# Kernel tuning notes

Hardware: AMD Instinct MI355X
Metric: run time of the kernel (lower is better)

The kernel has to match this reference:

```python
import jax, jax.numpy as jnp
import numpy as np

N_WAY = 100
K_SHOT = 10
N_SUPPORT = N_WAY * K_SHOT
N_QUERY = 8192
F_IN = 4096
D_EMB = 1024
EPS = 1e-6  # torch nn.PairwiseDistance default eps added to the difference


def setup_inputs() -> dict:
    key = jax.random.key(0)
    k1, k2, k3, k4 = jax.random.split(key, 4)
    support_images = jax.random.normal(k1, (N_SUPPORT, F_IN), dtype=jnp.float32)
    # dense labels 0..N_WAY-1, K_SHOT examples each (episodic sampling)
    support_labels = (jnp.arange(N_SUPPORT, dtype=jnp.int32) // K_SHOT)
    query_images = jax.random.normal(k2, (N_QUERY, F_IN), dtype=jnp.float32)
    W = jax.random.normal(k3, (F_IN, D_EMB), dtype=jnp.float32) * (1.0 / np.sqrt(F_IN))
    b = jax.random.normal(k4, (D_EMB,), dtype=jnp.float32) * 0.01
    return {"support_images": support_images, "support_labels": support_labels,
            "query_images": query_images, "W": W, "b": b}


def reference(support_images, support_labels, query_images, W, b):
    # backbone: linear feature extractor
    z_support = support_images @ W + b          # [N_SUPPORT, D]
    z_query = query_images @ W + b              # [N_QUERY, D]

    # group support embeddings by class (each class has exactly K_SHOT members)
    order = jnp.argsort(support_labels, stable=True)
    grouped = z_support[order].reshape(N_WAY, K_SHOT, D_EMB)  # [W, K, D]

    # torch .median(dim=0): lower median for even counts -> sorted[(K-1)//2]
    z_proto_med = jnp.sort(grouped, axis=1)[:, (K_SHOT - 1) // 2]  # [W, D]
    z_proto_mean = grouped.mean(axis=1)                            # [W, D]
    z_total = 0.5 * (z_proto_med + z_proto_mean)                   # [W, D]

    # pairwise L2 with torch PairwiseDistance eps: sqrt(sum((q - p + eps)^2))
    # expanded: ||q||^2 + ||p||^2 + D*eps^2 - 2 q.p + 2*eps*(sum q - sum p)
    q2 = jnp.sum(z_query * z_query, axis=-1, keepdims=True)       # [Q, 1]
    p2 = jnp.sum(z_total * z_total, axis=-1)[None, :]             # [1, W]
    qs = jnp.sum(z_query, axis=-1, keepdims=True)                 # [Q, 1]
    ps = jnp.sum(z_total, axis=-1)[None, :]                       # [1, W]
    cross = z_query @ z_total.T                                   # [Q, W]
    sq = q2 + p2 - 2.0 * cross + 2.0 * EPS * (qs - ps) + D_EMB * EPS * EPS
    dists = jnp.sqrt(jnp.maximum(sq, 0.0))                        # [Q, W]
    return -dists
```

## Files before the change

kernel.cpp:

```cpp
#include <hip/hip_runtime.h>


typedef unsigned short u16;
typedef __attribute__((ext_vector_type(4))) unsigned short u16x4;
typedef __attribute__((ext_vector_type(8))) unsigned short u16x8;
typedef __attribute__((ext_vector_type(8))) short bf16x8;
typedef __attribute__((ext_vector_type(4))) float f32x4;

#define N_QUERY 8192
#define F_IN    4096
#define D_EMB   1024
#define N_SUP   1000
#define N_WAY   100
#define BK      64
#define BM      96

__device__ __forceinline__ u16 f2b(float f) {
  unsigned int u = __builtin_bit_cast(unsigned int, f);
  u += 0x7FFFu + ((u >> 16) & 1u);
  return (u16)(u >> 16);
}
__device__ __forceinline__ float b2f(u16 u) {
  unsigned int x = ((unsigned int)u) << 16;
  return __builtin_bit_cast(float, x);
}

#define GLB_PTR(p) ((const __attribute__((address_space(1))) unsigned int*)(p))
#define LDS_PTR(p) ((__attribute__((address_space(3))) unsigned int*)(p))

__global__ __launch_bounds__(256) void wt_k(const float* __restrict__ W,
                                            u16* __restrict__ Wt) {
  __shared__ float tile[32][33];
  int kb = blockIdx.x * 32, nb = blockIdx.y * 32;
  int tx = threadIdx.x & 31, ty = threadIdx.x >> 5;
#pragma unroll
  for (int i = 0; i < 4; ++i) {
    int k = ty + i * 8;
    tile[k][tx] = W[(size_t)(kb + k) * D_EMB + nb + tx];
  }
  __syncthreads();
#pragma unroll
  for (int i = 0; i < 4; ++i) {
    int n = ty + i * 8;
    Wt[(size_t)(nb + n) * F_IN + kb + tx] = f2b(tile[tx][n]);
  }
}

__global__ __launch_bounds__(512) void gemm1_k(
    const float* __restrict__ qimg, const float* __restrict__ simg,
    const u16* __restrict__ Wt, const float* __restrict__ bias,
    u16* __restrict__ Zq) {
  __shared__ __align__(16) u16 As[BM * BK];
  __shared__ __align__(16) u16 Bs[128 * BK];
  const int tid  = threadIdx.x;
  const int lane = tid & 63, wid = tid >> 6;
  const int wr = wid >> 2, wc = wid & 3;
  int lin = blockIdx.x + (blockIdx.y << 3);
  int swz = (lin & 7) * 96 + (lin >> 3);
  const int rowBase = (swz >> 3) * BM;
  const int colBase = (swz & 7) * 128;
  const bool a2 = (tid < 256);

  const float* asrc[2];
  int aw[2];
#pragma unroll
  for (int i = 0; i < 2; ++i) {
    int g = i * 512 + tid;
    if (g > 767) g = 767;
    int row = g >> 3;
    int colb = ((g & 7) << 4) ^ ((row & 7) << 4);
    int grow = rowBase + row;
    int sr = grow - N_QUERY; if (sr < 0) sr = 0; if (sr > N_SUP - 1) sr = N_SUP - 1;
    const float* base = (grow < N_QUERY) ? qimg + (size_t)grow * F_IN
                                         : simg + (size_t)sr * F_IN;
    asrc[i] = base + (colb >> 1);
    aw[i] = g * 8;
  }
  const u16* bsrc[2];
  unsigned bldsoff[2];
#pragma unroll
  for (int i = 0; i < 2; ++i) {
    int g = i * 512 + tid;
    int n = g >> 3;
    int kb = ((g & 7) << 4) ^ ((n & 7) << 4);
    bsrc[i] = Wt + (size_t)(colBase + n) * F_IN + (kb >> 1);
    bldsoff[i] = i * 8192 + wid * 1024;
  }
  int aoff[3], boff[2];
#pragma unroll
  for (int m = 0; m < 3; ++m) {
    int row = wr * 48 + m * 16 + (lane & 15);
    aoff[m] = (row * 128 + (((lane >> 4) << 4) ^ ((row & 7) << 4))) >> 1;
  }
#pragma unroll
  for (int n = 0; n < 2; ++n) {
    int row = wc * 32 + n * 16 + (lane & 15);
    boff[n] = (row * 128 + (((lane >> 4) << 4) ^ ((row & 7) << 4))) >> 1;
  }

  f32x4 acc[3][2] = {};

#pragma unroll 1
  for (int kt = 0; kt < F_IN / BK; ++kt) {
    float4 v0a = *(const float4*)(asrc[0] + kt * BK);
    float4 v0b = *(const float4*)(asrc[0] + kt * BK + 4);
    float4 v1a = {}, v1b = {};
    if (a2) {
      v1a = *(const float4*)(asrc[1] + kt * BK);
      v1b = *(const float4*)(asrc[1] + kt * BK + 4);
    }
#pragma unroll
    for (int i = 0; i < 2; ++i)
      __builtin_amdgcn_global_load_lds(GLB_PTR(bsrc[i] + kt * BK),
                                       LDS_PTR((char*)Bs + bldsoff[i]), 16, 0, 0);
    u16x8 pk0 = { f2b(v0a.x), f2b(v0a.y), f2b(v0a.z), f2b(v0a.w),
                  f2b(v0b.x), f2b(v0b.y), f2b(v0b.z), f2b(v0b.w) };
    *(u16x8*)&As[aw[0]] = pk0;
    if (a2) {
      u16x8 pk1 = { f2b(v1a.x), f2b(v1a.y), f2b(v1a.z), f2b(v1a.w),
                    f2b(v1b.x), f2b(v1b.y), f2b(v1b.z), f2b(v1b.w) };
      *(u16x8*)&As[aw[1]] = pk1;
    }
    __syncthreads();

#pragma unroll
    for (int ks = 0; ks < 2; ++ks) {
      bf16x8 a[3], b[2];
#pragma unroll
      for (int m = 0; m < 3; ++m) a[m] = *(const bf16x8*)&As[aoff[m] ^ (ks << 5)];
#pragma unroll
      for (int n = 0; n < 2; ++n) b[n] = *(const bf16x8*)&Bs[boff[n] ^ (ks << 5)];
#pragma unroll
      for (int m = 0; m < 3; ++m)
#pragma unroll
        for (int n = 0; n < 2; ++n)
          acc[m][n] = __builtin_amdgcn_mfma_f32_16x16x32_bf16(a[m], b[n], acc[m][n], 0, 0, 0);
    }
    __syncthreads();
  }

#pragma unroll
  for (int n = 0; n < 2; ++n) {
    int c = colBase + wc * 32 + n * 16 + (lane & 15);
    float bvv = bias[c];
#pragma unroll
    for (int m = 0; m < 3; ++m) {
      int r0 = rowBase + wr * 48 + m * 16 + ((lane >> 4) * 4);
#pragma unroll
      for (int r = 0; r < 4; ++r)
        Zq[(size_t)(r0 + r) * D_EMB + c] = f2b(acc[m][n][r] + bvv);
    }
  }
}

__global__ __launch_bounds__(256) void proto_k(const u16* __restrict__ Zq,
                                               float* __restrict__ Ztf) {
  int gid = blockIdx.x * 256 + threadIdx.x;
  int w = gid >> 10, d = gid & 1023;
  float outv = 0.f;
  if (w < N_WAY) {
    float v[10]; float s = 0.f;
#pragma unroll
    for (int k = 0; k < 10; ++k) {
      v[k] = b2f(Zq[(size_t)(N_QUERY + w * 10 + k) * D_EMB + d]);
      s += v[k];
    }
#pragma unroll
    for (int a = 0; a < 9; ++a)
#pragma unroll
      for (int b2 = 0; b2 < 9; ++b2)
        if (b2 < 9 - a) {
          float lo = fminf(v[b2], v[b2 + 1]);
          float hi = fmaxf(v[b2], v[b2 + 1]);
          v[b2] = lo; v[b2 + 1] = hi;
        }
    outv = 0.5f * (v[4] + s * 0.1f);
  }
  Ztf[gid] = outv;
}

__global__ __launch_bounds__(256) void statsq_k(const u16* __restrict__ Zq,
                                                float* __restrict__ sum2,
                                                float* __restrict__ sum1) {
  int row = blockIdx.x;
  int t = threadIdx.x;
  u16x4 u = *(const u16x4*)(Zq + (size_t)row * D_EMB + t * 4);
  float x0 = b2f(u[0]), x1 = b2f(u[1]), x2 = b2f(u[2]), x3 = b2f(u[3]);
  float s  = x0 + x1 + x2 + x3;
  float s2 = x0 * x0 + x1 * x1 + x2 * x2 + x3 * x3;
#pragma unroll
  for (int o = 32; o > 0; o >>= 1) {
    s  += __shfl_down(s, o);
    s2 += __shfl_down(s2, o);
  }
  __shared__ float as1[4], as2[4];
  if ((t & 63) == 0) { as1[t >> 6] = s; as2[t >> 6] = s2; }
  __syncthreads();
  if (t == 0) {
    sum1[row] = as1[0] + as1[1] + as1[2] + as1[3];
    sum2[row] = as2[0] + as2[1] + as2[2] + as2[3];
  }
}

__global__ __launch_bounds__(256) void stats_k(const float* __restrict__ in,
                                               u16* __restrict__ outb,
                                               float* __restrict__ sum2,
                                               float* __restrict__ sum1) {
  int row = blockIdx.x;
  const float* r = in + (size_t)row * D_EMB;
  int t = threadIdx.x;
  float4 v = *(const float4*)(r + t * 4);
  u16x4 u4 = { f2b(v.x), f2b(v.y), f2b(v.z), f2b(v.w) };
  *(u16x4*)(outb + (size_t)row * D_EMB + t * 4) = u4;
  float s  = v.x + v.y + v.z + v.w;
  float s2 = v.x * v.x + v.y * v.y + v.z * v.z + v.w * v.w;
#pragma unroll
  for (int off = 32; off > 0; off >>= 1) {
    s  += __shfl_down(s, off);
    s2 += __shfl_down(s2, off);
  }
  __shared__ float as1[4], as2[4];
  if ((t & 63) == 0) { as1[t >> 6] = s; as2[t >> 6] = s2; }
  __syncthreads();
  if (t == 0) {
    sum1[row] = as1[0] + as1[1] + as1[2] + as1[3];
    sum2[row] = as2[0] + as2[1] + as2[2] + as2[3];
  }
}

#define LDA2 40
__global__ __launch_bounds__(256) void gemm2_k(
    const u16* __restrict__ Zq, const u16* __restrict__ Ztb,
    const float* __restrict__ q2, const float* __restrict__ qs,
    const float* __restrict__ p2, const float* __restrict__ ps,
    float* __restrict__ out) {
  __shared__ u16 As[64][LDA2];
  __shared__ u16 Bs[128][LDA2];
  const int tid = threadIdx.x;
  const int lane = tid & 63, wid = tid >> 6;
  const int wr = wid >> 1, wc = wid & 1;
  const int rowBase = blockIdx.x * 64;

  f32x4 acc[2][4] = {};

  for (int kt = 0; kt < D_EMB / 32; ++kt) {
    u16x8 avv;
    {
      int row = tid >> 2, kh = tid & 3;
      avv = *(const u16x8*)(Zq + (size_t)(rowBase + row) * D_EMB + kt * 32 + kh * 8);
    }
    u16x8 bvv[2];
#pragma unroll
    for (int i = 0; i < 2; ++i) {
      int u = i * 256 + tid;
      int n = u >> 2, kh = u & 3;
      bvv[i] = *(const u16x8*)(Ztb + (size_t)n * D_EMB + kt * 32 + kh * 8);
    }
    __syncthreads();
    {
      int row = tid >> 2, kh = tid & 3;
      *(u16x8*)&As[row][kh * 8] = avv;
    }
#pragma unroll
    for (int i = 0; i < 2; ++i) {
      int u = i * 256 + tid;
      int n = u >> 2, kh = u & 3;
      *(u16x8*)&Bs[n][kh * 8] = bvv[i];
    }
    __syncthreads();

    bf16x8 a[2], b[4];
#pragma unroll
    for (int m = 0; m < 2; ++m)
      a[m] = *(const bf16x8*)&As[wr * 32 + m * 16 + (lane & 15)][(lane >> 4) * 8];
#pragma unroll
    for (int n = 0; n < 4; ++n)
      b[n] = *(const bf16x8*)&Bs[wc * 64 + n * 16 + (lane & 15)][(lane >> 4) * 8];
#pragma unroll
    for (int m = 0; m < 2; ++m)
#pragma unroll
      for (int n = 0; n < 4; ++n)
        acc[m][n] = __builtin_amdgcn_mfma_f32_16x16x32_bf16(a[m], b[n], acc[m][n], 0, 0, 0);
    __syncthreads();
  }

#pragma unroll
  for (int m = 0; m < 2; ++m) {
    int r0 = rowBase + wr * 32 + m * 16 + ((lane >> 4) * 4);
    float q2v[4], qsv[4];
#pragma unroll
    for (int r = 0; r < 4; ++r) { q2v[r] = q2[r0 + r]; qsv[r] = qs[r0 + r]; }
#pragma unroll
    for (int n = 0; n < 4; ++n) {
      int c = wc * 64 + n * 16 + (lane & 15);
      if (c < N_WAY) {
        float pp = p2[c], pss = ps[c];
#pragma unroll
        for (int r = 0; r < 4; ++r) {
          float sq = q2v[r] + pp - 2.f * acc[m][n][r]
                   + 2e-6f * (qsv[r] - pss) + (float)D_EMB * 1e-12f;
          out[(size_t)(r0 + r) * N_WAY + c] = -sqrtf(fmaxf(sq, 0.f));
        }
      }
    }
  }
}

extern "C" void kernel_launch(void* const* d_in, const int* in_sizes, int n_in,
                              void* d_out, int out_size, void* d_ws, size_t ws_size,
                              hipStream_t stream) {
  const float* simg = (const float*)d_in[0];
  const float* qimg = (const float*)d_in[2];
  const float* W    = (const float*)d_in[3];
  const float* bias = (const float*)d_in[4];
  float* out = (float*)d_out;

  char* ws = (char*)d_ws;
  u16*   Wt  = (u16*)(ws);
  u16*   Zq  = (u16*)(ws + 8388608);
  float* Ztf = (float*)(ws + 27262976);
  u16*   Ztb = (u16*)(ws + 27787264);
  float* q2  = (float*)(ws + 28049408);
  float* qs  = (float*)(ws + 28082176);
  float* p2  = (float*)(ws + 28114944);
  float* ps  = (float*)(ws + 28115456);

  hipLaunchKernelGGL(wt_k,    dim3(128, 32), dim3(256), 0, stream, W, Wt);
  hipLaunchKernelGGL(gemm1_k, dim3(8, 96),   dim3(512), 0, stream, qimg, simg, Wt, bias, Zq);
  hipLaunchKernelGGL(proto_k, dim3(512),     dim3(256), 0, stream, Zq, Ztf);
  hipLaunchKernelGGL(statsq_k, dim3(8192),   dim3(256), 0, stream, Zq, q2, qs);
  hipLaunchKernelGGL(stats_k, dim3(128),     dim3(256), 0, stream, Ztf, Ztb, p2, ps);
  hipLaunchKernelGGL(gemm2_k, dim3(128),     dim3(256), 0, stream, Zq, Ztb, q2, qs, p2, ps, out);
}
```

Baseline: 144.3 us.

## Fuse query norm/sum stats into distance GEMM and halve its row tile

Drops the separate statsq_k kernel and computes each query row's sum and sum of squares inside gemm2_k from the A tiles it already loads, reducing across the four lanes per row through shared memory. The GEMM row tile is halved from 64 to 32 so the grid doubles to 256 blocks for better CU coverage. This removes one launch and a full re-read of Zq. In exchange, half the threads sit idle during A loads and the B tile is reloaded twice as often across blocks.

```diff
diff --git a/kernel.cpp b/kernel.cpp
--- a/kernel.cpp
+++ b/kernel.cpp
@@ -179,29 +179,6 @@
   Ztf[gid] = outv;
 }
 
-__global__ __launch_bounds__(256) void statsq_k(const u16* __restrict__ Zq,
-                                                float* __restrict__ sum2,
-                                                float* __restrict__ sum1) {
-  int row = blockIdx.x;
-  int t = threadIdx.x;
-  u16x4 u = *(const u16x4*)(Zq + (size_t)row * D_EMB + t * 4);
-  float x0 = b2f(u[0]), x1 = b2f(u[1]), x2 = b2f(u[2]), x3 = b2f(u[3]);
-  float s  = x0 + x1 + x2 + x3;
-  float s2 = x0 * x0 + x1 * x1 + x2 * x2 + x3 * x3;
-#pragma unroll
-  for (int o = 32; o > 0; o >>= 1) {
-    s  += __shfl_down(s, o);
-    s2 += __shfl_down(s2, o);
-  }
-  __shared__ float as1[4], as2[4];
-  if ((t & 63) == 0) { as1[t >> 6] = s; as2[t >> 6] = s2; }
-  __syncthreads();
-  if (t == 0) {
-    sum1[row] = as1[0] + as1[1] + as1[2] + as1[3];
-    sum2[row] = as2[0] + as2[1] + as2[2] + as2[3];
-  }
-}
-
 __global__ __launch_bounds__(256) void stats_k(const float* __restrict__ in,
                                                u16* __restrict__ outb,
                                                float* __restrict__ sum2,
@@ -231,21 +208,23 @@
 #define LDA2 40
 __global__ __launch_bounds__(256) void gemm2_k(
     const u16* __restrict__ Zq, const u16* __restrict__ Ztb,
-    const float* __restrict__ q2, const float* __restrict__ qs,
     const float* __restrict__ p2, const float* __restrict__ ps,
     float* __restrict__ out) {
-  __shared__ u16 As[64][LDA2];
+  __shared__ u16 As[32][LDA2];
   __shared__ u16 Bs[128][LDA2];
+  __shared__ float q2_l[32], qs_l[32];
   const int tid = threadIdx.x;
   const int lane = tid & 63, wid = tid >> 6;
   const int wr = wid >> 1, wc = wid & 1;
-  const int rowBase = blockIdx.x * 64;
-
-  f32x4 acc[2][4] = {};
+  const int rowBase = blockIdx.x * 32;
+  const bool stA = (tid < 128);
+
+  f32x4 acc[4] = {};
+  float rs = 0.f, rs2 = 0.f;
 
   for (int kt = 0; kt < D_EMB / 32; ++kt) {
-    u16x8 avv;
-    {
+    u16x8 avv = {};
+    if (stA) {
       int row = tid >> 2, kh = tid & 3;
       avv = *(const u16x8*)(Zq + (size_t)(rowBase + row) * D_EMB + kt * 32 + kh * 8);
     }
@@ -257,9 +236,14 @@
       bvv[i] = *(const u16x8*)(Ztb + (size_t)n * D_EMB + kt * 32 + kh * 8);
     }
     __syncthreads();
-    {
+    if (stA) {
       int row = tid >> 2, kh = tid & 3;
       *(u16x8*)&As[row][kh * 8] = avv;
+#pragma unroll
+      for (int j = 0; j < 8; ++j) {
+        float x = b2f(avv[j]);
+        rs += x; rs2 += x * x;
+      }
     }
 #pragma unroll
     for (int i = 0; i < 2; ++i) {
@@ -269,27 +253,30 @@
     }
     __syncthreads();
 
-    bf16x8 a[2], b[4];
-#pragma unroll
-    for (int m = 0; m < 2; ++m)
-      a[m] = *(const bf16x8*)&As[wr * 32 + m * 16 + (lane & 15)][(lane >> 4) * 8];
+    bf16x8 a, b[4];
+    a = *(const bf16x8*)&As[wr * 16 + (lane & 15)][(lane >> 4) * 8];
 #pragma unroll
     for (int n = 0; n < 4; ++n)
       b[n] = *(const bf16x8*)&Bs[wc * 64 + n * 16 + (lane & 15)][(lane >> 4) * 8];
 #pragma unroll
-    for (int m = 0; m < 2; ++m)
-#pragma unroll
-      for (int n = 0; n < 4; ++n)
-        acc[m][n] = __builtin_amdgcn_mfma_f32_16x16x32_bf16(a[m], b[n], acc[m][n], 0, 0, 0);
-    __syncthreads();
-  }
-
-#pragma unroll
-  for (int m = 0; m < 2; ++m) {
-    int r0 = rowBase + wr * 32 + m * 16 + ((lane >> 4) * 4);
+    for (int n = 0; n < 4; ++n)
+      acc[n] = __builtin_amdgcn_mfma_f32_16x16x32_bf16(a, b[n], acc[n], 0, 0, 0);
+    __syncthreads();
+  }
+
+  rs  += __shfl_down(rs, 1);  rs  += __shfl_down(rs, 2);
+  rs2 += __shfl_down(rs2, 1); rs2 += __shfl_down(rs2, 2);
+  if (stA && (tid & 3) == 0) {
+    qs_l[tid >> 2] = rs;
+    q2_l[tid >> 2] = rs2;
+  }
+  __syncthreads();
+
+  {
+    int r0 = wr * 16 + ((lane >> 4) * 4);
     float q2v[4], qsv[4];
 #pragma unroll
-    for (int r = 0; r < 4; ++r) { q2v[r] = q2[r0 + r]; qsv[r] = qs[r0 + r]; }
+    for (int r = 0; r < 4; ++r) { q2v[r] = q2_l[r0 + r]; qsv[r] = qs_l[r0 + r]; }
 #pragma unroll
     for (int n = 0; n < 4; ++n) {
       int c = wc * 64 + n * 16 + (lane & 15);
@@ -297,9 +284,9 @@
         float pp = p2[c], pss = ps[c];
 #pragma unroll
         for (int r = 0; r < 4; ++r) {
-          float sq = q2v[r] + pp - 2.f * acc[m][n][r]
+          float sq = q2v[r] + pp - 2.f * acc[n][r]
                    + 2e-6f * (qsv[r] - pss) + (float)D_EMB * 1e-12f;
-          out[(size_t)(r0 + r) * N_WAY + c] = -sqrtf(fmaxf(sq, 0.f));
+          out[(size_t)(rowBase + r0 + r) * N_WAY + c] = -sqrtf(fmaxf(sq, 0.f));
         }
       }
     }
@@ -320,15 +307,12 @@
   u16*   Zq  = (u16*)(ws + 8388608);
   float* Ztf = (float*)(ws + 27262976);
   u16*   Ztb = (u16*)(ws + 27787264);
-  float* q2  = (float*)(ws + 28049408);
-  float* qs  = (float*)(ws + 28082176);
   float* p2  = (float*)(ws + 28114944);
   float* ps  = (float*)(ws + 28115456);
 
   hipLaunchKernelGGL(wt_k,    dim3(128, 32), dim3(256), 0, stream, W, Wt);
   hipLaunchKernelGGL(gemm1_k, dim3(8, 96),   dim3(512), 0, stream, qimg, simg, Wt, bias, Zq);
   hipLaunchKernelGGL(proto_k, dim3(512),     dim3(256), 0, stream, Zq, Ztf);
-  hipLaunchKernelGGL(statsq_k, dim3(8192),   dim3(256), 0, stream, Zq, q2, qs);
   hipLaunchKernelGGL(stats_k, dim3(128),     dim3(256), 0, stream, Ztf, Ztb, p2, ps);
-  hipLaunchKernelGGL(gemm2_k, dim3(128),     dim3(256), 0, stream, Zq, Ztb, q2, qs, p2, ps, out);
-}
+  hipLaunchKernelGGL(gemm2_k, dim3(256),     dim3(256), 0, stream, Zq, Ztb, p2, ps, out);
+}
```

After: 139.2 us. 1.04x faster.
